# Optimization experiments

Hardware: AMD Instinct MI355X
Metric: run time of the kernel (lower is better)

## Reference

```python
import jax, jax.numpy as jnp
import numpy as np

B, L, S = 128, 400, 30
V, EMB, H, M, OOV = 50000, 128, 512, 512, 30


def setup_inputs():
    ks = jax.random.split(jax.random.key(0), 32)
    rn = lambda k, s, sc=0.05: jax.random.normal(k, s, dtype=jnp.float32) * sc
    return {
        "h": rn(ks[0], (1, B, H), 1.0),
        "word_memory_bank": rn(ks[1], (B, L, M), 1.0),
        "sent_memory_bank": rn(ks[2], (B, S, M), 1.0),
        "src_word_mask": (jax.random.uniform(ks[3], (B, L)) < 0.9).astype(jnp.float32),
        "src_sent_mask": (jax.random.uniform(ks[4], (B, S)) < 0.9).astype(jnp.float32),
        "coverage": jnp.zeros((B, L), jnp.float32),
        "emb_table": rn(ks[5], (V, EMB), 1.0).at[0].set(0.0),  # pad_idx=0 row zeroed
        "gru_w_ih": rn(ks[6], (3 * H, EMB)),
        "gru_w_hh": rn(ks[7], (3 * H, H)),
        "gru_b_ih": rn(ks[8], (3 * H,)),
        "gru_b_hh": rn(ks[9], (3 * H,)),
        "w_mem_proj": rn(ks[10], (H, M)),
        "w_dec_proj_w": rn(ks[11], (H, H)),
        "w_dec_proj_b": rn(ks[12], (H,)),
        "w_v": rn(ks[13], (H,)),
        "w_cov_proj": rn(ks[14], (H,)),
        "s_mem_proj": rn(ks[15], (H, M)),
        "s_dec_proj_w": rn(ks[16], (H, H)),
        "s_dec_proj_b": rn(ks[17], (H,)),
        "s_v": rn(ks[18], (H,)),
        "pgen_w": rn(ks[19], (EMB + H + 2 * M,)),
        "pgen_b": rn(ks[20], (1,)),
        "vd1_w": rn(ks[21], (H, H + 2 * M)),
        "vd1_b": rn(ks[22], (H,)),
        "vd2_w": rn(ks[23], (V, H)),
        "vd2_b": rn(ks[24], (V,)),
        "y": jax.random.randint(ks[25], (B,), 0, V),
        "src_oov": jax.random.randint(ks[26], (B, L), 0, V + OOV),
        "max_num_oovs": OOV,
    }


def _attn_concat(dec, mem, mask, mem_proj, dec_w, dec_b, v, cov=None, cov_proj=None):
    # concat/Bahdanau attention: score = v^T tanh(W_m m + W_d s [+ W_c c])
    feat = jnp.einsum('blm,dm->bld', mem, mem_proj) + (dec @ dec_w.T + dec_b)[:, None, :]
    if cov is not None:
        feat = feat + cov[:, :, None] * cov_proj[None, None, :]
    scores = jnp.einsum('bld,d->bl', jnp.tanh(feat), v)
    attn = jax.nn.softmax(scores, axis=1)
    if mask is not None:  # masked softmax: softmax, mask, renormalize
        attn = attn * mask
        attn = attn / (jnp.sum(attn, axis=1, keepdims=True) + 1e-10)
    ctx = jnp.einsum('bl,blm->bm', attn, mem)
    new_cov = cov + attn if cov is not None else None
    return ctx, attn, new_cov


def _forward(h, word_memory_bank, sent_memory_bank, src_word_mask, src_sent_mask,
             coverage, emb_table, gru_w_ih, gru_w_hh, gru_b_ih, gru_b_hh,
             w_mem_proj, w_dec_proj_w, w_dec_proj_b, w_v, w_cov_proj,
             s_mem_proj, s_dec_proj_w, s_dec_proj_b, s_v,
             pgen_w, pgen_b, vd1_w, vd1_b, vd2_w, vd2_b, y, src_oov, max_num_oovs):
    bsz = src_oov.shape[0]
    y_emb = emb_table[y]  # [B, EMB]
    # single-step GRU (PyTorch gate layout r,z,n)
    gi = y_emb @ gru_w_ih.T + gru_b_ih
    gh = h[-1] @ gru_w_hh.T + gru_b_hh
    ir, iz, inn = jnp.split(gi, 3, axis=1)
    hr, hz, hn = jnp.split(gh, 3, axis=1)
    r = jax.nn.sigmoid(ir + hr)
    z = jax.nn.sigmoid(iz + hz)
    n = jnp.tanh(inn + r * hn)
    h_last = (1.0 - z) * n + z * h[-1]  # [B, H]
    h_next = h_last[None]  # [1, B, H]
    word_ctx, word_attn, word_cov = _attn_concat(
        h_last, word_memory_bank, src_word_mask, w_mem_proj, w_dec_proj_w,
        w_dec_proj_b, w_v, coverage, w_cov_proj)
    sent_ctx, _, _ = _attn_concat(
        h_last, sent_memory_bank, src_sent_mask, s_mem_proj, s_dec_proj_w,
        s_dec_proj_b, s_v)
    context = jnp.concatenate([word_ctx, sent_ctx], axis=1)  # [B, 2M]
    hid = jnp.concatenate([context, h_last], axis=1) @ vd1_w.T + vd1_b
    vocab_dist = jax.nn.softmax(hid @ vd2_w.T + vd2_b, axis=1)  # [B, V]
    pg_in = jnp.concatenate([context, h_last, y_emb], axis=1)
    p_gen = jax.nn.sigmoid(pg_in @ pgen_w + pgen_b)[:, None]  # [B, 1]
    vocab_dist_ = p_gen * vocab_dist
    attn_dist_ = (1.0 - p_gen) * word_attn
    vocab_dist_ = jnp.concatenate(
        [vocab_dist_, jnp.zeros((bsz, max_num_oovs), vocab_dist_.dtype)], axis=1)
    final_dist = vocab_dist_.at[jnp.arange(bsz)[:, None], src_oov].add(attn_dist_)
    return final_dist, h_next, word_ctx, word_attn, p_gen, word_cov


def reference(h, word_memory_bank, sent_memory_bank, src_word_mask, src_sent_mask,
              coverage, emb_table, gru_w_ih, gru_w_hh, gru_b_ih, gru_b_hh,
              w_mem_proj, w_dec_proj_w, w_dec_proj_b, w_v, w_cov_proj,
              s_mem_proj, s_dec_proj_w, s_dec_proj_b, s_v,
              pgen_w, pgen_b, vd1_w, vd1_b, vd2_w, vd2_b, y, src_oov, max_num_oovs):
    return _forward(h, word_memory_bank, sent_memory_bank, src_word_mask,
                    src_sent_mask, coverage, emb_table, gru_w_ih, gru_w_hh,
                    gru_b_ih, gru_b_hh, w_mem_proj, w_dec_proj_w, w_dec_proj_b,
                    w_v, w_cov_proj, s_mem_proj, s_dec_proj_w, s_dec_proj_b,
                    s_v, pgen_w, pgen_b, vd1_w, vd1_b, vd2_w, vd2_b,
                    y, src_oov, max_num_oovs)
```

## Files before the change

### kernel.cpp

```cpp
#include <hip/hip_runtime.h>
#include <hip/hip_bf16.h>
#include <math.h>

#define B 128
#define L 400
#define S 30
#define V 50000
#define EMB 128
#define H 512
#define M 512
#define OOV 30
#define H3 1536
#define VO (V + OOV)
#define NTILE 391
#define NPART (2 * NTILE)
#define PSTRIDE 800

#define O_HN    (B * VO)
#define O_WCTX  (O_HN + B * H)
#define O_WATTN (O_WCTX + B * M)
#define O_PGEN  (O_WATTN + B * L)
#define O_WCOV  (O_PGEN + B)

typedef short bf16x8 __attribute__((ext_vector_type(8)));
typedef float f32x4 __attribute__((ext_vector_type(4)));

__device__ __forceinline__ unsigned pk2(float a, float b) {
    union { __hip_bfloat162 h; unsigned u; } cv;
    cv.h = __float22bfloat162_rn(make_float2(a, b));
    return cv.u;
}

__device__ __forceinline__ float fast_tanh(float x) {
    float e = __expf(2.f * x);
    return 1.f - 2.f * __builtin_amdgcn_rcpf(e + 1.f);
}

__global__ void k_setup(const float* __restrict__ bih, const float* __restrict__ bhh,
                        const float* __restrict__ bdpw, const float* __restrict__ bdps,
                        const float* __restrict__ v1b, const float* __restrict__ emb,
                        const int* __restrict__ y,
                        float* gi, float* gh, float* dpw, float* dps, float* hid,
                        float* wscore, float* sscore, float* yemb,
                        const float* __restrict__ wih, const float* __restrict__ whh,
                        const float* __restrict__ wdpw, const float* __restrict__ wdps,
                        const float* __restrict__ wmpw, const float* __restrict__ wmps,
                        const float* __restrict__ v1,
                        short* o_ih, short* o_hh, short* o_dpw, short* o_dps,
                        short* o_mpw, short* o_mps, short* o_v1) {
    int bb = blockIdx.x;
    if (bb < 2583) {
        int i = bb * 256 + threadIdx.x;
        if (i < 196608) { gi[i] = bih[i % 1536]; return; }
        i -= 196608;
        if (i < 196608) { gh[i] = bhh[i % 1536]; return; }
        i -= 196608;
        if (i < 65536) { dpw[i] = bdpw[i & 511]; return; }
        i -= 65536;
        if (i < 65536) { dps[i] = bdps[i & 511]; return; }
        i -= 65536;
        if (i < 65536) { hid[i] = v1b[i & 511]; return; }
        i -= 65536;
        if (i < 51200) { wscore[i] = 0.f; return; }
        i -= 51200;
        if (i < 3840) { sscore[i] = 0.f; return; }
        i -= 3840;
        if (i < 16384) { int b = i >> 7, e = i & 127; yemb[i] = emb[(size_t)y[b] * EMB + e]; }
        return;
    }
    bb -= 2583;
    const float* src; short* dst;
    if      (bb < 96)  { src = wih;  dst = o_ih; }
    else if (bb < 480) { src = whh;  dst = o_hh;  bb -= 96; }
    else if (bb < 608) { src = wdpw; dst = o_dpw; bb -= 480; }
    else if (bb < 736) { src = wdps; dst = o_dps; bb -= 608; }
    else if (bb < 864) { src = wmpw; dst = o_mpw; bb -= 736; }
    else if (bb < 992) { src = wmps; dst = o_mps; bb -= 864; }
    else               { src = v1;   dst = o_v1;  bb -= 992; }
    size_t i = (size_t)bb * 2048 + threadIdx.x * 8;
    float4 a = *(const float4*)(src + i);
    float4 c = *(const float4*)(src + i + 4);
    uint4 w;
    w.x = pk2(a.x, a.y); w.y = pk2(a.z, a.w);
    w.z = pk2(c.x, c.y); w.w = pk2(c.z, c.w);
    *(uint4*)(dst + i) = w;
}

__device__ __forceinline__ void stage_a(const float* __restrict__ src, int SK, int rmax,
                                        int t, short dst[128][72]) {
    int col = (t & 7) * 8;
    int r0 = t >> 3;
#pragma unroll
    for (int i = 0; i < 4; ++i) {
        int r = r0 + i * 32;
        int rr = r < rmax ? r : rmax;
        const float* p = src + (size_t)rr * SK + col;
        float4 a = *(const float4*)p;
        float4 c = *(const float4*)(p + 4);
        uint4 w;
        w.x = pk2(a.x, a.y); w.y = pk2(a.z, a.w);
        w.z = pk2(c.x, c.y); w.w = pk2(c.z, c.w);
        *(uint4*)&dst[r][col] = w;
    }
}

__device__ __forceinline__ void stage_b128bf(const short* __restrict__ src, int K,
                                             int t, short dst[128][72]) {
    int col = (t & 7) * 8;
    int r0 = t >> 3;
#pragma unroll
    for (int i = 0; i < 4; ++i) {
        int r = r0 + i * 32;
        *(bf16x8*)&dst[r][col] = *(const bf16x8*)(src + (size_t)r * K + col);
    }
}

__device__ __forceinline__ void stage_sw(const float* __restrict__ src, int SK, int rmax,
                                         int t, short* __restrict__ dst) {
    int c8 = t & 7, r0 = t >> 3;
#pragma unroll
    for (int i = 0; i < 4; ++i) {
        int r = r0 + i * 32;
        int rr = r < rmax ? r : rmax;
        const float* p = src + (size_t)rr * SK + c8 * 8;
        float4 a = *(const float4*)p;
        float4 c = *(const float4*)(p + 4);
        uint4 w;
        w.x = pk2(a.x, a.y); w.y = pk2(a.z, a.w);
        w.z = pk2(c.x, c.y); w.w = pk2(c.z, c.w);
        int q = c8 ^ (r & 7);
        *(uint4*)&dst[(r * 8 + q) * 8] = w;
    }
}

__global__ __launch_bounds__(256, 2) void k_mmsk(
        const float* __restrict__ A0, const short* __restrict__ B0, float* __restrict__ C0,
        int K0, int NT0, int KB0,
        const float* __restrict__ A1, const short* __restrict__ B1, float* __restrict__ C1,
        int K1, int NT1, int KB1) {
    __shared__ short As[128][72];
    __shared__ short Bs[128][72];
    int t = threadIdx.x, lane = t & 63, wv = t >> 6;
    int wr = wv >> 1, wc = wv & 1;
    int l15 = lane & 15, l4 = lane >> 4;

    int bb = blockIdx.x;
    const float* A; const short* Bb; float* C; int K, NT, KB;
    if (bb < NT0 * KB0) { A = A0; Bb = B0; C = C0; K = K0; NT = NT0; KB = KB0; }
    else { bb -= NT0 * KB0; A = A1; Bb = B1; C = C1; K = K1; NT = NT1; KB = KB1; }
    int nIdx = bb % NT, kIdx = bb / NT;
    int ldc = NT * 128;
    int nBase = nIdx * 128;
    int KC = K / KB;
    int kLo = kIdx * KC, kHi = kLo + KC;

    f32x4 acc[4][4] = {};
    for (int kc = kLo; kc < kHi; kc += 64) {
        stage_a(A + kc, K, 127, t, As);
        stage_b128bf(Bb + (size_t)nBase * K + kc, K, t, Bs);
        __syncthreads();
#pragma unroll
        for (int kk = 0; kk < 2; ++kk) {
            bf16x8 af[4], bq[4];
#pragma unroll
            for (int i = 0; i < 4; ++i)
                af[i] = *(const bf16x8*)&As[wr * 64 + i * 16 + l15][kk * 32 + l4 * 8];
#pragma unroll
            for (int j = 0; j < 4; ++j)
                bq[j] = *(const bf16x8*)&Bs[wc * 64 + j * 16 + l15][kk * 32 + l4 * 8];
#pragma unroll
            for (int i = 0; i < 4; ++i)
#pragma unroll
                for (int j = 0; j < 4; ++j)
                    acc[i][j] = __builtin_amdgcn_mfma_f32_16x16x32_bf16(
                        af[i], bq[j], acc[i][j], 0, 0, 0);
        }
        __syncthreads();
    }
#pragma unroll
    for (int i = 0; i < 4; ++i)
#pragma unroll
        for (int r = 0; r < 4; ++r) {
            int row = wr * 64 + i * 16 + l4 * 4 + r;
#pragma unroll
            for (int j = 0; j < 4; ++j) {
                int n = nBase + wc * 64 + j * 16 + l15;
                atomicAdd(&C[(size_t)row * ldc + n], acc[i][j][r]);
            }
        }
}

__global__ __launch_bounds__(256, 4) void k_mm128(
        const float* __restrict__ Ap, const float* __restrict__ Bf,
        const float* __restrict__ bias, float* __restrict__ C,
        float* __restrict__ pm, float* __restrict__ ps) {
    __shared__ short As[128 * 64];
    __shared__ short Bs[128 * 64];
    int t = threadIdx.x, lane = t & 63, wv = t >> 6;
    int wr = wv >> 1, wc = wv & 1;
    int l15 = lane & 15, l4 = lane >> 4;
    int nBase = blockIdx.x * 128;
    int brmax = V - 1 - nBase; if (brmax > 127) brmax = 127;
    int swz = l15 & 7;

    f32x4 acc[4][4] = {};
    for (int kc = 0; kc < H; kc += 64) {
        stage_sw(Ap + kc, H, 127, t, As);
        stage_sw(Bf + (size_t)nBase * H + kc, H, brmax, t, Bs);
        __syncthreads();
#pragma unroll
        for (int kk = 0; kk < 2; ++kk) {
            int q = (kk * 4 + l4) ^ swz;
            bf16x8 af[4], bq[4];
#pragma unroll
            for (int i = 0; i < 4; ++i)
                af[i] = *(const bf16x8*)&As[((wr * 64 + i * 16 + l15) * 8 + q) * 8];
#pragma unroll
            for (int j = 0; j < 4; ++j)
                bq[j] = *(const bf16x8*)&Bs[((wc * 64 + j * 16 + l15) * 8 + q) * 8];
#pragma unroll
            for (int i = 0; i < 4; ++i)
#pragma unroll
                for (int j = 0; j < 4; ++j)
                    acc[i][j] = __builtin_amdgcn_mfma_f32_16x16x32_bf16(
                        af[i], bq[j], acc[i][j], 0, 0, 0);
        }
        __syncthreads();
    }
#pragma unroll
    for (int i = 0; i < 4; ++i)
#pragma unroll
        for (int r = 0; r < 4; ++r) {
            int row = wr * 64 + i * 16 + l4 * 4 + r;
            float val[4];
            float mrow = -3e38f;
#pragma unroll
            for (int j = 0; j < 4; ++j) {
                int n = nBase + wc * 64 + j * 16 + l15;
                val[j] = acc[i][j][r] + bias[n < V ? n : 0];
                if (n < V) {
                    C[(size_t)row * V + n] = val[j];
                    mrow = fmaxf(mrow, val[j]);
                }
            }
            float srow = 0.f;
#pragma unroll
            for (int j = 0; j < 4; ++j) {
                int n = nBase + wc * 64 + j * 16 + l15;
                if (n < V) srow += __expf(val[j] - mrow);
            }
#pragma unroll
            for (int off = 1; off < 16; off <<= 1) {
                float mo = __shfl_xor(mrow, off, 16), so = __shfl_xor(srow, off, 16);
                float mn = fmaxf(mrow, mo);
                srow = srow * __expf(mrow - mn) + so * __expf(mo - mn);
                mrow = mn;
            }
            if (l15 == 0) {
                int idx = blockIdx.x * 2 + wc;
                pm[row * PSTRIDE + idx] = mrow;
                ps[row * PSTRIDE + idx] = srow;
            }
        }
}

__global__ __launch_bounds__(1024, 4) void k_feat(
        const float* __restrict__ wmb, const short* __restrict__ wbmpw,
        const float* __restrict__ dpw, const float* __restrict__ cov,
        const float* __restrict__ covp, const float* __restrict__ vw,
        float* __restrict__ wscore,
        const float* __restrict__ smb, const short* __restrict__ wbmps,
        const float* __restrict__ dps, const float* __restrict__ vs,
        float* __restrict__ sscore) {
    __shared__ short As[128 * 64];
    __shared__ short Bs[512 * 64];
    int t = threadIdx.x, lane = t & 63, wv = t >> 6;
    int wr = wv >> 3, wc = wv & 7;
    int l15 = lane & 15, l4 = lane >> 4;
    int swz = l15 & 7;

    bool word = blockIdx.x < 400;
    const float* Ap; const short* Bbf; const float* dproj; const float* vvec; float* outp;
    int rowBase;
    if (word) { Ap = wmb; Bbf = wbmpw; dproj = dpw; vvec = vw; outp = wscore; rowBase = blockIdx.x * 128; }
    else      { Ap = smb; Bbf = wbmps; dproj = dps; vvec = vs; outp = sscore; rowBase = (blockIdx.x - 400) * 128; }
    const float* Asrc = Ap + (size_t)rowBase * 512;

    int c8 = t & 7;
    int r0 = t >> 3;

    float4 pa[2];
    auto loadA = [&](int kc) {
        const float* p = Asrc + (size_t)r0 * 512 + kc * 64 + c8 * 8;
        pa[0] = *(const float4*)p;
        pa[1] = *(const float4*)(p + 4);
    };

    f32x4 acc[4][4] = {};
    loadA(0);
    for (int kc = 0; kc < 8; ++kc) {
        bf16x8 pb[4];
#pragma unroll
        for (int i = 0; i < 4; ++i)
            pb[i] = *(const bf16x8*)(Bbf + (size_t)(r0 + i * 128) * 512 + kc * 64 + c8 * 8);
        {
            uint4 w;
            w.x = pk2(pa[0].x, pa[0].y); w.y = pk2(pa[0].z, pa[0].w);
            w.z = pk2(pa[1].x, pa[1].y); w.w = pk2(pa[1].z, pa[1].w);
            *(uint4*)&As[(r0 * 8 + (c8 ^ (r0 & 7))) * 8] = w;
        }
#pragma unroll
        for (int i = 0; i < 4; ++i) {
            int r = r0 + i * 128;
            *(bf16x8*)&Bs[(r * 8 + (c8 ^ (r & 7))) * 8] = pb[i];
        }
        __syncthreads();
        if (kc < 7) loadA(kc + 1);
#pragma unroll
        for (int kk = 0; kk < 2; ++kk) {
            bf16x8 af[4], bq[4];
#pragma unroll
            for (int i = 0; i < 4; ++i) {
                int R = wr * 64 + i * 16 + l15;
                af[i] = *(const bf16x8*)&As[(R * 8 + ((kk * 4 + l4) ^ (R & 7))) * 8];
            }
#pragma unroll
            for (int j = 0; j < 4; ++j) {
                int C = wc * 64 + j * 16 + l15;
                bq[j] = *(const bf16x8*)&Bs[(C * 8 + ((kk * 4 + l4) ^ (C & 7))) * 8];
            }
#pragma unroll
            for (int i = 0; i < 4; ++i)
#pragma unroll
                for (int j = 0; j < 4; ++j)
                    acc[i][j] = __builtin_amdgcn_mfma_f32_16x16x32_bf16(
                        af[i], bq[j], acc[i][j], 0, 0, 0);
        }
        __syncthreads();
    }
    int dB = wc * 64;
    float vv[4], cp[4], dp0[4], dp1[4];
    int b0 = word ? rowBase / 400 : 0;
    int b1 = word ? (rowBase + 127) / 400 : 0;
#pragma unroll
    for (int j = 0; j < 4; ++j) {
        int d = dB + j * 16 + l15;
        vv[j] = vvec[d];
        cp[j] = word ? covp[d] : 0.f;
        if (word) { dp0[j] = dproj[b0 * H + d]; dp1[j] = dproj[b1 * H + d]; }
    }
#pragma unroll
    for (int i = 0; i < 4; ++i) {
#pragma unroll
        for (int r = 0; r < 4; ++r) {
            int row = rowBase + wr * 64 + i * 16 + l4 * 4 + r;
            int b = word ? (row / 400) : (row / 30);
            float cv = word ? cov[row] : 0.f;
            bool use0 = (b == b0);
            float s = 0.f;
#pragma unroll
            for (int j = 0; j < 4; ++j) {
                float dpv = word ? (use0 ? dp0[j] : dp1[j])
                                 : dproj[b * H + dB + j * 16 + l15];
                float f = acc[i][j][r] + dpv + cv * cp[j];
                s += vv[j] * fast_tanh(f);
            }
            s += __shfl_xor(s, 8, 16);
            s += __shfl_xor(s, 4, 16);
            s += __shfl_xor(s, 2, 16);
            s += __shfl_xor(s, 1, 16);
            if (l15 == 0) atomicAdd(&outp[row], s);
        }
    }
}

__global__ void k_gates(const float* __restrict__ gi, const float* __restrict__ gh,
                        const float* __restrict__ h, float* __restrict__ hnext) {
    int i = blockIdx.x * 256 + threadIdx.x;
    int b = i >> 9, k = i & 511;
    float ir = gi[b * H3 + k], iz = gi[b * H3 + H + k], inn = gi[b * H3 + 2 * H + k];
    float hr = gh[b * H3 + k], hz = gh[b * H3 + H + k], hn = gh[b * H3 + 2 * H + k];
    float r = 1.f / (1.f + __expf(-(ir + hr)));
    float z = 1.f / (1.f + __expf(-(iz + hz)));
    float n = fast_tanh(inn + r * hn);
    hnext[i] = (1.f - z) * n + z * h[i];
}

__global__ __launch_bounds__(256) void k_smax_sent(
        const float* __restrict__ wscore, const float* __restrict__ wmask,
        const float* __restrict__ cov, float* __restrict__ wattn, float* __restrict__ wcov,
        const float* __restrict__ sscore, const float* __restrict__ smask,
        const float* __restrict__ smb, float* __restrict__ sctx) {
    __shared__ float sc[L];
    __shared__ float red[4];
    int t = threadIdx.x;
    if (blockIdx.x < B) {
        int b = blockIdx.x;
        float mx = -1e30f;
        for (int l = t; l < L; l += 256) { float s = wscore[b * L + l]; sc[l] = s; mx = fmaxf(mx, s); }
        for (int off = 32; off; off >>= 1) mx = fmaxf(mx, __shfl_xor(mx, off));
        if ((t & 63) == 0) red[t >> 6] = mx;
        __syncthreads();
        mx = fmaxf(fmaxf(red[0], red[1]), fmaxf(red[2], red[3]));
        __syncthreads();
        float sm = 0.f;
        for (int l = t; l < L; l += 256) { float e = __expf(sc[l] - mx); sc[l] = e; sm += e; }
        for (int off = 32; off; off >>= 1) sm += __shfl_xor(sm, off);
        if ((t & 63) == 0) red[t >> 6] = sm;
        __syncthreads();
        float Z = red[0] + red[1] + red[2] + red[3];
        __syncthreads();
        float sm2 = 0.f;
        for (int l = t; l < L; l += 256) {
            float a = (sc[l] / Z) * wmask[b * L + l];
            sc[l] = a; sm2 += a;
        }
        for (int off = 32; off; off >>= 1) sm2 += __shfl_xor(sm2, off);
        if ((t & 63) == 0) red[t >> 6] = sm2;
        __syncthreads();
        float Zm = red[0] + red[1] + red[2] + red[3] + 1e-10f;
        for (int l = t; l < L; l += 256) {
            float a = sc[l] / Zm;
            wattn[b * L + l] = a;
            wcov[b * L + l] = cov[b * L + l] + a;
        }
    } else {
        int b = blockIdx.x - B;
        float* sa = sc; float* sa2 = sc + 32; float* smk = sc + 64;
        if (t < S) { sa[t] = sscore[b * S + t]; smk[t] = smask[b * S + t]; }
        __syncthreads();
        if (t < S) {
            float mx = -1e30f;
            for (int l = 0; l < S; ++l) mx = fmaxf(mx, sa[l]);
            float Z = 0.f, Zm = 0.f;
            for (int l = 0; l < S; ++l) { float e = __expf(sa[l] - mx); Z += e; Zm += e * smk[l]; }
            float e = __expf(sa[t] - mx);
            float a = (e / Z) * smk[t];
            sa2[t] = a / (Zm / Z + 1e-10f);
        }
        __syncthreads();
        float a0 = 0.f, a1 = 0.f;
        for (int l = 0; l < S; ++l) {
            const float* r = smb + ((size_t)b * S + l) * M;
            float a = sa2[l];
            a0 += a * r[t]; a1 += a * r[t + 256];
        }
        sctx[b * M + t] = a0; sctx[b * M + t + 256] = a1;
    }
}

__global__ __launch_bounds__(256) void k_ctx_part(
        const float* __restrict__ attn, const float* __restrict__ memb,
        float* __restrict__ ctxp) {
    __shared__ float sa[100];
    int b = blockIdx.y, ch = blockIdx.x, t = threadIdx.x;
    int l0 = ch * 100;
    if (t < 100) sa[t] = attn[b * L + l0 + t];
    __syncthreads();
    float ax = 0.f, ay = 0.f;
    const float* base = memb + ((size_t)b * L + l0) * M + t * 2;
#pragma unroll 4
    for (int l = 0; l < 100; ++l) {
        float2 m2 = *(const float2*)(base + (size_t)l * M);
        float a = sa[l];
        ax += a * m2.x; ay += a * m2.y;
    }
    float* o = ctxp + ((size_t)(ch * B + b)) * M + t * 2;
    o[0] = ax; o[1] = ay;
}

__global__ void k_ctxcat(const float* __restrict__ ctxp, const float* __restrict__ sctx,
                         const float* __restrict__ hnext, const float* __restrict__ yemb,
                         const float* __restrict__ pw, const float* __restrict__ pb,
                         float* __restrict__ wctx, float* __restrict__ cat,
                         float* __restrict__ pg) {
    int bb = blockIdx.x, t = threadIdx.x;
    if (bb < 256) {
        int j = bb * 256 + t;
        float v = ctxp[j] + ctxp[B * M + j] + ctxp[2 * B * M + j] + ctxp[3 * B * M + j];
        wctx[j] = v;
        int b = j >> 9, c = j & 511;
        cat[b * H3 + c] = v;
    } else if (bb < 768) {
        int i = (bb - 256) * 256 + t;
        int b = i >> 10, c = i & 1023;
        cat[b * H3 + 512 + c] = (c < 512) ? sctx[b * 512 + c] : hnext[b * 512 + c - 512];
    } else {
        int b = bb - 768;
        if (t < 64) {
            float s = 0.f;
            for (int i = t; i < EMB + H + 2 * M; i += 64) {
                float x;
                if (i < 512) {
                    int j = b * 512 + i;
                    x = ctxp[j] + ctxp[B * M + j] + ctxp[2 * B * M + j] + ctxp[3 * B * M + j];
                } else if (i < 1024) x = sctx[b * 512 + i - 512];
                else if (i < 1536)   x = hnext[b * 512 + i - 1024];
                else                 x = yemb[b * EMB + i - 1536];
                s += x * pw[i];
            }
            for (int off = 32; off; off >>= 1) s += __shfl_xor(s, off);
            if (t == 0) pg[b] = 1.f / (1.f + __expf(-(s + pb[0])));
        }
    }
}

__global__ __launch_bounds__(256) void k_vwrite(
        const float* __restrict__ logits, const float* __restrict__ pm,
        const float* __restrict__ ps, const float* __restrict__ pgen,
        float* __restrict__ fd) {
    __shared__ float wm[4], wsv[4];
    int b = blockIdx.y, t = threadIdx.x;
    float m = -3e38f, s = 0.f;
    for (int i = t; i < NPART; i += 256) {
        float mo = pm[b * PSTRIDE + i], so = ps[b * PSTRIDE + i];
        float mn = fmaxf(m, mo);
        s = s * __expf(m - mn) + so * __expf(mo - mn);
        m = mn;
    }
    for (int off = 32; off; off >>= 1) {
        float mo = __shfl_xor(m, off), so = __shfl_xor(s, off);
        float mn = fmaxf(m, mo);
        s = s * __expf(m - mn) + so * __expf(mo - mn);
        m = mn;
    }
    if ((t & 63) == 0) { wm[t >> 6] = m; wsv[t >> 6] = s; }
    __syncthreads();
    float M2 = fmaxf(fmaxf(wm[0], wm[1]), fmaxf(wm[2], wm[3]));
    float S2 = wsv[0] * __expf(wm[0] - M2) + wsv[1] * __expf(wm[1] - M2) +
               wsv[2] * __expf(wm[2] - M2) + wsv[3] * __expf(wm[3] - M2);
    float inv = pgen[b] / S2;
    int col0 = blockIdx.x * 2048 + t * 8;
    float* outb = fd + (size_t)b * VO;
    if (col0 + 8 <= V) {
        const float4* lp = (const float4*)(logits + (size_t)b * V + col0);
        float4 x = lp[0], z = lp[1];
        *(float2*)(outb + col0)     = make_float2(inv * __expf(x.x - M2), inv * __expf(x.y - M2));
        *(float2*)(outb + col0 + 2) = make_float2(inv * __expf(x.z - M2), inv * __expf(x.w - M2));
        *(float2*)(outb + col0 + 4) = make_float2(inv * __expf(z.x - M2), inv * __expf(z.y - M2));
        *(float2*)(outb + col0 + 6) = make_float2(inv * __expf(z.z - M2), inv * __expf(z.w - M2));
    } else {
#pragma unroll
        for (int k = 0; k < 8; k += 2) {
            int c = col0 + k;
            if (c + 2 <= VO) {
                float2 o;
                o.x = (c < V)     ? inv * __expf(logits[(size_t)b * V + c] - M2) : 0.f;
                o.y = (c + 1 < V) ? inv * __expf(logits[(size_t)b * V + c + 1] - M2) : 0.f;
                *(float2*)(outb + c) = o;
            }
        }
    }
}

__global__ void k_scatter(const int* __restrict__ oov, const float* __restrict__ wattn,
                          const float* __restrict__ pgen, float* __restrict__ fd) {
    int i = blockIdx.x * 256 + threadIdx.x;
    int b = i / L;
    float w = (1.f - pgen[b]) * wattn[i];
    atomicAdd(&fd[(size_t)b * VO + oov[i]], w);
}

extern "C" void kernel_launch(void* const* d_in, const int* in_sizes, int n_in,
                              void* d_out, int out_size, void* d_ws, size_t ws_size,
                              hipStream_t stream) {
    const float* h     = (const float*)d_in[0];
    const float* wmb   = (const float*)d_in[1];
    const float* smb   = (const float*)d_in[2];
    const float* wmask = (const float*)d_in[3];
    const float* smask = (const float*)d_in[4];
    const float* cov   = (const float*)d_in[5];
    const float* emb   = (const float*)d_in[6];
    const float* Wih   = (const float*)d_in[7];
    const float* Whh   = (const float*)d_in[8];
    const float* bih   = (const float*)d_in[9];
    const float* bhh   = (const float*)d_in[10];
    const float* Wmpw  = (const float*)d_in[11];
    const float* Wdpw  = (const float*)d_in[12];
    const float* bdpw  = (const float*)d_in[13];
    const float* vw    = (const float*)d_in[14];
    const float* covp  = (const float*)d_in[15];
    const float* Wmps  = (const float*)d_in[16];
    const float* Wdps  = (const float*)d_in[17];
    const float* bdps  = (const float*)d_in[18];
    const float* vs    = (const float*)d_in[19];
    const float* pw    = (const float*)d_in[20];
    const float* pb    = (const float*)d_in[21];
    const float* vd1w  = (const float*)d_in[22];
    const float* vd1b  = (const float*)d_in[23];
    const float* vd2w  = (const float*)d_in[24];
    const float* vd2b  = (const float*)d_in[25];
    const int*   y     = (const int*)d_in[26];
    const int*   oov   = (const int*)d_in[27];

    float* out   = (float*)d_out;
    float* fd    = out;
    float* hnext = out + O_HN;
    float* wctx  = out + O_WCTX;
    float* wattn = out + O_WATTN;
    float* pgen  = out + O_PGEN;
    float* wcov  = out + O_WCOV;

    float* ws     = (float*)d_ws;
    float* yemb   = ws;
    float* gi     = yemb + B * EMB;
    float* gh     = gi + B * H3;
    float* dpw    = gh + B * H3;
    float* dps    = dpw + B * H;
    float* wscore = dps + B * H;
    float* sscore = wscore + B * L;
    float* sctx   = sscore + B * S;
    float* hid    = sctx + B * M;
    float* logits = hid + B * H;
    float* cat    = gi;
    float* ctxp   = logits;
    short* wb     = (short*)(logits + (size_t)B * V);
    short* wb_ih  = wb;
    short* wb_hh  = wb_ih + H3 * EMB;
    short* wb_dpw = wb_hh + H3 * H;
    short* wb_dps = wb_dpw + H * H;
    short* wb_mpw = wb_dps + H * H;
    short* wb_mps = wb_mpw + H * M;
    short* wb_v1  = wb_mps + H * M;
    float* pm     = (float*)(wb_v1 + H * H3);
    float* psum   = pm + B * PSTRIDE;

    k_setup<<<2583 + 1376, 256, 0, stream>>>(bih, bhh, bdpw, bdps, vd1b, emb, y,
                                             gi, gh, dpw, dps, hid, wscore, sscore, yemb,
                                             Wih, Whh, Wdpw, Wdps, Wmpw, Wmps, vd1w,
                                             wb_ih, wb_hh, wb_dpw, wb_dps, wb_mpw, wb_mps, wb_v1);
    k_mmsk<<<36, 256, 0, stream>>>(yemb, wb_ih, gi, 128, 12, 1,
                                   h, wb_hh, gh, 512, 12, 2);
    k_gates<<<256, 256, 0, stream>>>(gi, gh, h, hnext);
    k_mmsk<<<16, 256, 0, stream>>>(hnext, wb_dpw, dpw, 512, 4, 2,
                                   hnext, wb_dps, dps, 512, 4, 2);
    k_feat<<<430, 1024, 0, stream>>>(wmb, wb_mpw, dpw, cov, covp, vw, wscore,
                                     smb, wb_mps, dps, vs, sscore);
    k_smax_sent<<<2 * B, 256, 0, stream>>>(wscore, wmask, cov, wattn, wcov,
                                           sscore, smask, smb, sctx);
    k_ctx_part<<<dim3(4, B), 256, 0, stream>>>(wattn, wmb, ctxp);
    k_ctxcat<<<768 + B, 256, 0, stream>>>(ctxp, sctx, hnext, yemb, pw, pb,
                                          wctx, cat, pgen);
    k_mmsk<<<24, 256, 0, stream>>>(cat, wb_v1, hid, 1536, 4, 6,
                                   nullptr, nullptr, nullptr, 64, 1, 0);
    k_mm128<<<NTILE, 256, 0, stream>>>(hid, vd2w, vd2b, logits, pm, psum);
    k_vwrite<<<dim3(25, B), 256, 0, stream>>>(logits, pm, psum, pgen, fd);
    k_scatter<<<200, 256, 0, stream>>>(oov, wattn, pgen, fd);
}
```

Baseline: 228.5 us.

## Load matmul operands straight from global into registers, double-buffer A tile

In the vocab-projection kernel k_mm128, both operands are now read straight from global memory into MFMA fragment registers and converted to bf16 on the fly. This removes the LDS staging and the block barriers. In k_feat, the B weight fragments are likewise read directly from global memory. The A tile there moves to a double-buffered LDS scheme that prefetches two steps ahead and needs one barrier per k-step. Launch-bounds occupancy hints are relaxed as well. The trade-off is that global loads are now uncoalesced per-lane loads that rely on cache reuse, and fragments may be loaded redundantly across waves.

```diff
diff --git a/kernel.cpp b/kernel.cpp
--- a/kernel.cpp
+++ b/kernel.cpp
@@ -29,6 +29,13 @@
     union { __hip_bfloat162 h; unsigned u; } cv;
     cv.h = __float22bfloat162_rn(make_float2(a, b));
     return cv.u;
+}
+
+__device__ __forceinline__ bf16x8 cvt8(float4 a, float4 b) {
+    union { unsigned u[4]; bf16x8 v; } r;
+    r.u[0] = pk2(a.x, a.y); r.u[1] = pk2(a.z, a.w);
+    r.u[2] = pk2(b.x, b.y); r.u[3] = pk2(b.z, b.w);
+    return r.v;
 }
 
 __device__ __forceinline__ float fast_tanh(float x) {
@@ -115,24 +122,6 @@
     }
 }
 
-__device__ __forceinline__ void stage_sw(const float* __restrict__ src, int SK, int rmax,
-                                         int t, short* __restrict__ dst) {
-    int c8 = t & 7, r0 = t >> 3;
-#pragma unroll
-    for (int i = 0; i < 4; ++i) {
-        int r = r0 + i * 32;
-        int rr = r < rmax ? r : rmax;
-        const float* p = src + (size_t)rr * SK + c8 * 8;
-        float4 a = *(const float4*)p;
-        float4 c = *(const float4*)(p + 4);
-        uint4 w;
-        w.x = pk2(a.x, a.y); w.y = pk2(a.z, a.w);
-        w.z = pk2(c.x, c.y); w.w = pk2(c.z, c.w);
-        int q = c8 ^ (r & 7);
-        *(uint4*)&dst[(r * 8 + q) * 8] = w;
-    }
-}
-
 __global__ __launch_bounds__(256, 2) void k_mmsk(
         const float* __restrict__ A0, const short* __restrict__ B0, float* __restrict__ C0,
         int K0, int NT0, int KB0,
@@ -190,34 +179,39 @@
         }
 }
 
-__global__ __launch_bounds__(256, 4) void k_mm128(
+__global__ __launch_bounds__(256) void k_mm128(
         const float* __restrict__ Ap, const float* __restrict__ Bf,
         const float* __restrict__ bias, float* __restrict__ C,
         float* __restrict__ pm, float* __restrict__ ps) {
-    __shared__ short As[128 * 64];
-    __shared__ short Bs[128 * 64];
     int t = threadIdx.x, lane = t & 63, wv = t >> 6;
     int wr = wv >> 1, wc = wv & 1;
     int l15 = lane & 15, l4 = lane >> 4;
     int nBase = blockIdx.x * 128;
-    int brmax = V - 1 - nBase; if (brmax > 127) brmax = 127;
-    int swz = l15 & 7;
+
+    const float* Abase = Ap + (size_t)(wr * 64 + l15) * 512 + l4 * 8;
+    int n0 = nBase + wc * 64 + l15;
+    const float* Bb0 = Bf + (size_t)(n0 < V ? n0 : V - 1) * 512 + l4 * 8;
+    const float* Bb1 = Bf + (size_t)(n0 + 16 < V ? n0 + 16 : V - 1) * 512 + l4 * 8;
+    const float* Bb2 = Bf + (size_t)(n0 + 32 < V ? n0 + 32 : V - 1) * 512 + l4 * 8;
+    const float* Bb3 = Bf + (size_t)(n0 + 48 < V ? n0 + 48 : V - 1) * 512 + l4 * 8;
 
     f32x4 acc[4][4] = {};
-    for (int kc = 0; kc < H; kc += 64) {
-        stage_sw(Ap + kc, H, 127, t, As);
-        stage_sw(Bf + (size_t)nBase * H + kc, H, brmax, t, Bs);
-        __syncthreads();
+    for (int kc = 0; kc < 8; ++kc) {
 #pragma unroll
         for (int kk = 0; kk < 2; ++kk) {
-            int q = (kk * 4 + l4) ^ swz;
+            int ko = kc * 64 + kk * 32;
             bf16x8 af[4], bq[4];
 #pragma unroll
-            for (int i = 0; i < 4; ++i)
-                af[i] = *(const bf16x8*)&As[((wr * 64 + i * 16 + l15) * 8 + q) * 8];
-#pragma unroll
-            for (int j = 0; j < 4; ++j)
-                bq[j] = *(const bf16x8*)&Bs[((wc * 64 + j * 16 + l15) * 8 + q) * 8];
+            for (int i = 0; i < 4; ++i) {
+                const float* p = Abase + (size_t)(i * 16) * 512 + ko;
+                af[i] = cvt8(*(const float4*)p, *(const float4*)(p + 4));
+            }
+            {
+                const float* p0 = Bb0 + ko; bq[0] = cvt8(*(const float4*)p0, *(const float4*)(p0 + 4));
+                const float* p1 = Bb1 + ko; bq[1] = cvt8(*(const float4*)p1, *(const float4*)(p1 + 4));
+                const float* p2 = Bb2 + ko; bq[2] = cvt8(*(const float4*)p2, *(const float4*)(p2 + 4));
+                const float* p3 = Bb3 + ko; bq[3] = cvt8(*(const float4*)p3, *(const float4*)(p3 + 4));
+            }
 #pragma unroll
             for (int i = 0; i < 4; ++i)
 #pragma unroll
@@ -225,7 +219,6 @@
                     acc[i][j] = __builtin_amdgcn_mfma_f32_16x16x32_bf16(
                         af[i], bq[j], acc[i][j], 0, 0, 0);
         }
-        __syncthreads();
     }
 #pragma unroll
     for (int i = 0; i < 4; ++i)
@@ -264,7 +257,7 @@
         }
 }
 
-__global__ __launch_bounds__(1024, 4) void k_feat(
+__global__ __launch_bounds__(1024) void k_feat(
         const float* __restrict__ wmb, const short* __restrict__ wbmpw,
         const float* __restrict__ dpw, const float* __restrict__ cov,
         const float* __restrict__ covp, const float* __restrict__ vw,
@@ -272,12 +265,10 @@
         const float* __restrict__ smb, const short* __restrict__ wbmps,
         const float* __restrict__ dps, const float* __restrict__ vs,
         float* __restrict__ sscore) {
-    __shared__ short As[128 * 64];
-    __shared__ short Bs[512 * 64];
+    __shared__ short As[2][128 * 64];
     int t = threadIdx.x, lane = t & 63, wv = t >> 6;
     int wr = wv >> 3, wc = wv & 7;
     int l15 = lane & 15, l4 = lane >> 4;
-    int swz = l15 & 7;
 
     bool word = blockIdx.x < 400;
     const float* Ap; const short* Bbf; const float* dproj; const float* vvec; float* outp;
@@ -285,49 +276,41 @@
     if (word) { Ap = wmb; Bbf = wbmpw; dproj = dpw; vvec = vw; outp = wscore; rowBase = blockIdx.x * 128; }
     else      { Ap = smb; Bbf = wbmps; dproj = dps; vvec = vs; outp = sscore; rowBase = (blockIdx.x - 400) * 128; }
     const float* Asrc = Ap + (size_t)rowBase * 512;
+    const short* Bsrc = Bbf + (size_t)(wc * 64 + l15) * 512 + l4 * 8;
 
     int c8 = t & 7;
     int r0 = t >> 3;
-
-    float4 pa[2];
+    int wslot = (r0 * 8 + (c8 ^ (r0 & 7))) * 8;
+
+    float4 pa0, pa1;
     auto loadA = [&](int kc) {
         const float* p = Asrc + (size_t)r0 * 512 + kc * 64 + c8 * 8;
-        pa[0] = *(const float4*)p;
-        pa[1] = *(const float4*)(p + 4);
+        pa0 = *(const float4*)p;
+        pa1 = *(const float4*)(p + 4);
     };
+    auto writeA = [&](int buf) {
+        uint4 w;
+        w.x = pk2(pa0.x, pa0.y); w.y = pk2(pa0.z, pa0.w);
+        w.z = pk2(pa1.x, pa1.y); w.w = pk2(pa1.z, pa1.w);
+        *(uint4*)&As[buf][wslot] = w;
+    };
 
     f32x4 acc[4][4] = {};
-    loadA(0);
+    loadA(0); writeA(0); loadA(1);
+    __syncthreads();
     for (int kc = 0; kc < 8; ++kc) {
-        bf16x8 pb[4];
-#pragma unroll
-        for (int i = 0; i < 4; ++i)
-            pb[i] = *(const bf16x8*)(Bbf + (size_t)(r0 + i * 128) * 512 + kc * 64 + c8 * 8);
-        {
-            uint4 w;
-            w.x = pk2(pa[0].x, pa[0].y); w.y = pk2(pa[0].z, pa[0].w);
-            w.z = pk2(pa[1].x, pa[1].y); w.w = pk2(pa[1].z, pa[1].w);
-            *(uint4*)&As[(r0 * 8 + (c8 ^ (r0 & 7))) * 8] = w;
-        }
-#pragma unroll
-        for (int i = 0; i < 4; ++i) {
-            int r = r0 + i * 128;
-            *(bf16x8*)&Bs[(r * 8 + (c8 ^ (r & 7))) * 8] = pb[i];
-        }
-        __syncthreads();
-        if (kc < 7) loadA(kc + 1);
+        const short* Bk = Bsrc + kc * 64;
 #pragma unroll
         for (int kk = 0; kk < 2; ++kk) {
-            bf16x8 af[4], bq[4];
+            bf16x8 bq[4];
+#pragma unroll
+            for (int j = 0; j < 4; ++j)
+                bq[j] = *(const bf16x8*)(Bk + (size_t)(j * 16) * 512 + kk * 32);
+            bf16x8 af[4];
 #pragma unroll
             for (int i = 0; i < 4; ++i) {
                 int R = wr * 64 + i * 16 + l15;
-                af[i] = *(const bf16x8*)&As[(R * 8 + ((kk * 4 + l4) ^ (R & 7))) * 8];
-            }
-#pragma unroll
-            for (int j = 0; j < 4; ++j) {
-                int C = wc * 64 + j * 16 + l15;
-                bq[j] = *(const bf16x8*)&Bs[(C * 8 + ((kk * 4 + l4) ^ (C & 7))) * 8];
+                af[i] = *(const bf16x8*)&As[kc & 1][(R * 8 + ((kk * 4 + l4) ^ (R & 7))) * 8];
             }
 #pragma unroll
             for (int i = 0; i < 4; ++i)
@@ -335,6 +318,10 @@
                 for (int j = 0; j < 4; ++j)
                     acc[i][j] = __builtin_amdgcn_mfma_f32_16x16x32_bf16(
                         af[i], bq[j], acc[i][j], 0, 0, 0);
+        }
+        if (kc < 7) {
+            writeA((kc + 1) & 1);
+            if (kc < 6) loadA(kc + 2);
         }
         __syncthreads();
     }
```

Result: slower. 276.2 us (+20.9%).

## Stage full A tile in LDS once and read B fragments directly from global

Applied to the files above, without the earlier changes.

The feature-projection GEMM kernel now loads the entire 128x512 A tile (converted to bf16) into shared memory up front with a single barrier. B operand fragments are read straight from global memory (L2-cached) instead of being staged through LDS, which removes the per-k-chunk double barrier loop. The occupancy hint in launch bounds is relaxed. This trades LDS staging and synchronisation for more global/L2 traffic on B and less latency hiding on A loads.

```diff
diff --git a/kernel.cpp b/kernel.cpp
--- a/kernel.cpp
+++ b/kernel.cpp
@@ -264,7 +264,7 @@
         }
 }
 
-__global__ __launch_bounds__(1024, 4) void k_feat(
+__global__ __launch_bounds__(1024) void k_feat(
         const float* __restrict__ wmb, const short* __restrict__ wbmpw,
         const float* __restrict__ dpw, const float* __restrict__ cov,
         const float* __restrict__ covp, const float* __restrict__ vw,
@@ -272,12 +272,10 @@
         const float* __restrict__ smb, const short* __restrict__ wbmps,
         const float* __restrict__ dps, const float* __restrict__ vs,
         float* __restrict__ sscore) {
-    __shared__ short As[128 * 64];
-    __shared__ short Bs[512 * 64];
+    __shared__ short As[128 * 512];
     int t = threadIdx.x, lane = t & 63, wv = t >> 6;
     int wr = wv >> 3, wc = wv & 7;
     int l15 = lane & 15, l4 = lane >> 4;
-    int swz = l15 & 7;
 
     bool word = blockIdx.x < 400;
     const float* Ap; const short* Bbf; const float* dproj; const float* vvec; float* outp;
@@ -286,58 +284,46 @@
     else      { Ap = smb; Bbf = wbmps; dproj = dps; vvec = vs; outp = sscore; rowBase = (blockIdx.x - 400) * 128; }
     const float* Asrc = Ap + (size_t)rowBase * 512;
 
-    int c8 = t & 7;
-    int r0 = t >> 3;
-
-    float4 pa[2];
-    auto loadA = [&](int kc) {
-        const float* p = Asrc + (size_t)r0 * 512 + kc * 64 + c8 * 8;
-        pa[0] = *(const float4*)p;
-        pa[1] = *(const float4*)(p + 4);
-    };
-
+    {
+        int r = t >> 3, gs = t & 7;
+        const float* arow = Asrc + (size_t)r * 512;
+#pragma unroll
+        for (int k = 0; k < 8; ++k) {
+            int g = gs + 8 * k;
+            const float* p = arow + g * 8;
+            float4 a0 = *(const float4*)p;
+            float4 a1 = *(const float4*)(p + 4);
+            uint4 w;
+            w.x = pk2(a0.x, a0.y); w.y = pk2(a0.z, a0.w);
+            w.z = pk2(a1.x, a1.y); w.w = pk2(a1.z, a1.w);
+            *(uint4*)&As[((size_t)r * 64 + (g ^ (r & 15))) * 8] = w;
+        }
+    }
+    __syncthreads();
+
+    const short* Bsrc = Bbf + (size_t)(wc * 64 + l15) * 512 + l4 * 8;
     f32x4 acc[4][4] = {};
-    loadA(0);
-    for (int kc = 0; kc < 8; ++kc) {
-        bf16x8 pb[4];
+#pragma unroll
+    for (int ko = 0; ko < 16; ++ko) {
+        bf16x8 bq[4];
+#pragma unroll
+        for (int j = 0; j < 4; ++j)
+            bq[j] = *(const bf16x8*)(Bsrc + (size_t)(j * 16) * 512 + ko * 32);
+        bf16x8 af[4];
+        int g = ko * 4 + l4;
+#pragma unroll
+        for (int i = 0; i < 4; ++i) {
+            int R = wr * 64 + i * 16 + l15;
+            af[i] = *(const bf16x8*)&As[((size_t)R * 64 + (g ^ (R & 15))) * 8];
+        }
 #pragma unroll
         for (int i = 0; i < 4; ++i)
-            pb[i] = *(const bf16x8*)(Bbf + (size_t)(r0 + i * 128) * 512 + kc * 64 + c8 * 8);
-        {
-            uint4 w;
-            w.x = pk2(pa[0].x, pa[0].y); w.y = pk2(pa[0].z, pa[0].w);
-            w.z = pk2(pa[1].x, pa[1].y); w.w = pk2(pa[1].z, pa[1].w);
-            *(uint4*)&As[(r0 * 8 + (c8 ^ (r0 & 7))) * 8] = w;
-        }
-#pragma unroll
-        for (int i = 0; i < 4; ++i) {
-            int r = r0 + i * 128;
-            *(bf16x8*)&Bs[(r * 8 + (c8 ^ (r & 7))) * 8] = pb[i];
-        }
-        __syncthreads();
-        if (kc < 7) loadA(kc + 1);
-#pragma unroll
-        for (int kk = 0; kk < 2; ++kk) {
-            bf16x8 af[4], bq[4];
-#pragma unroll
-            for (int i = 0; i < 4; ++i) {
-                int R = wr * 64 + i * 16 + l15;
-                af[i] = *(const bf16x8*)&As[(R * 8 + ((kk * 4 + l4) ^ (R & 7))) * 8];
-            }
-#pragma unroll
-            for (int j = 0; j < 4; ++j) {
-                int C = wc * 64 + j * 16 + l15;
-                bq[j] = *(const bf16x8*)&Bs[(C * 8 + ((kk * 4 + l4) ^ (C & 7))) * 8];
-            }
-#pragma unroll
-            for (int i = 0; i < 4; ++i)
-#pragma unroll
-                for (int j = 0; j < 4; ++j)
-                    acc[i][j] = __builtin_amdgcn_mfma_f32_16x16x32_bf16(
-                        af[i], bq[j], acc[i][j], 0, 0, 0);
-        }
-        __syncthreads();
-    }
+#pragma unroll
+            for (int j = 0; j < 4; ++j)
+                acc[i][j] = __builtin_amdgcn_mfma_f32_16x16x32_bf16(
+                    af[i], bq[j], acc[i][j], 0, 0, 0);
+    }
+
     int dB = wc * 64;
     float vv[4], cp[4], dp0[4], dp1[4];
     int b0 = word ? rowBase / 400 : 0;
```

After: 268.4 us. +17.5%, slower.
